# Optimization experiments

Hardware: AMD Instinct MI355X
Metric: run time of the kernel (lower is better)

The kernel has to match this reference:

```python
import jax, jax.numpy as jnp
import numpy as np

B, C, RXD, E, P, OSIZE = 64, 4, 64, 512, 4, 256


def setup_inputs() -> dict:
    key = jax.random.key(0)
    ks = jax.random.split(key, 6)
    x = jax.random.normal(ks[0], (B, C, RXD, E), dtype=jnp.float32)
    # rxd permutation (gather form of the one-hot permuteRxdMatrix matmul)
    rxd_perm = jax.random.permutation(ks[1], RXD)
    # E permutation and its compositions: permuter = permuter @ permuteEMatrix
    # in column-index form: idx_{p+1}[j] = idx_p[e_perm[j]]
    e_perm = np.array(jax.random.permutation(ks[2], E))
    idx = e_perm.copy()
    cols = []
    for _ in range(P):
        cols.append(idx.copy())
        idx = idx[e_perm]
    e_idx = jnp.asarray(np.stack(cols, axis=1))  # (E, P) int
    # sign selected at the single nonzero entry of each permutation column
    signs = (jax.random.uniform(ks[3], (E, P)) > 0.5).astype(jnp.float32) * 2.0 - 1.0
    fan_in = RXD * E * P
    W = jax.random.normal(ks[4], (OSIZE, fan_in), dtype=jnp.float32) / np.float32(np.sqrt(fan_in))
    b = jax.random.normal(ks[5], (OSIZE,), dtype=jnp.float32) * 0.01
    return {"x": x, "rxd_perm": rxd_perm, "e_idx": e_idx, "signs": signs, "W": W, "b": b}


def reference(x, rxd_perm, e_idx, signs, W, b):
    Bb, Cc, R, Ee = x.shape
    Pp = e_idx.shape[1]
    # permute rxd axis (exact equivalent of x.transpose @ one-hot matrix)
    out = x[:, :, rxd_perm, :]                      # (B,C,R,E)
    # signed E-permutations for all P powers (exact equiv of dense matmul
    # with permuteETensor * signTensor, which has one signed nonzero per column)
    out = out[..., e_idx] * signs                   # (B,C,R,E,P)
    L = R * Ee
    pieces = []
    for p in range(Pp):
        k = 2 ** p
        v = out[..., p].reshape(Bb, Cc, L)
        if k == 1:
            pieces.append(v)                        # pool+unpool with k=1 is identity
        else:
            Lp = ((L + k - 1) // k) * k             # ceil_mode padding
            vp = jnp.pad(v, ((0, 0), (0, 0), (0, Lp - L)), constant_values=-jnp.inf)
            w = vp.reshape(Bb, Cc, Lp // k, k)
            am = jnp.argmax(w, axis=-1)             # first max, matching torch MaxPool1d
            mx = jnp.max(w, axis=-1)
            onehot = jnp.arange(k) == am[..., None]
            # MaxUnpool: max value at argmax position, zeros elsewhere
            pieces.append(jnp.where(onehot, mx[..., None], 0.0).reshape(Bb, Cc, Lp))
    pieces[-1] = pieces[-1][:, :, :L]               # truncate last piece to L
    cat = jnp.concatenate(pieces, axis=2)           # (B,C,L*P) since L % k == 0
    return cat @ W.T + b                            # (B,C,OSIZE)
```

## Files before the change

### kernel.cpp

```cpp
#include <hip/hip_runtime.h>
#include <stdint.h>

#define B_ 64
#define C_ 4
#define R_ 64
#define E_ 512
#define P_ 4
#define OS_ 256
#define L_ (R_*E_)
#define K_ (L_*P_)
#define M_ (B_*C_)

#define BM 128
#define BN 128
#define BK 32
#define KCH 2048
#define AS_STR 40
#define WS_STR 36

typedef float  floatx4 __attribute__((ext_vector_type(4)));
typedef short  shortx8 __attribute__((ext_vector_type(8)));

static __device__ __forceinline__ unsigned short f2bf(float f) {
  union { float f; unsigned int u; } v; v.f = f;
  unsigned int u = v.u;
  u += 0x7fffu + ((u >> 16) & 1u);
  return (unsigned short)(u >> 16);
}

__global__ __launch_bounds__(512) void build_A(
    const float* __restrict__ x, const int* __restrict__ rxd_perm,
    const int* __restrict__ e_idx, const float* __restrict__ signs,
    unsigned short* __restrict__ A) {
  const int bcr = blockIdx.x;
  const int r  = bcr & (R_ - 1);
  const int bc = bcr >> 6;
  const int e  = threadIdx.x;
  __shared__ float xr[E_];
  __shared__ float vbuf[E_];
  const int pr = rxd_perm[r];
  xr[e] = x[((size_t)bc * R_ + pr) * E_ + e];
  __syncthreads();
  #pragma unroll
  for (int p = 0; p < P_; ++p) {
    const float v = xr[e_idx[e * P_ + p]] * signs[e * P_ + p];
    vbuf[e] = v;
    __syncthreads();
    float outv = v;
    if (p > 0) {
      const int k = 1 << p;
      const int base = e & ~(k - 1);
      float m = vbuf[base]; int am = base;
      for (int j = 1; j < k; ++j) {
        float t = vbuf[base + j];
        if (t > m) { m = t; am = base + j; }
      }
      outv = (e == am) ? v : 0.0f;
    }
    A[(size_t)bc * K_ + (size_t)p * L_ + r * E_ + e] = f2bf(outv);
    __syncthreads();
  }
}

__global__ void init_out(const float* __restrict__ bias, float* __restrict__ out) {
  const int i = blockIdx.x * blockDim.x + threadIdx.x;
  out[i] = bias[i & (OS_ - 1)];
}

__global__ __launch_bounds__(256) void gemm_splitk(
    const unsigned short* __restrict__ A, const float* __restrict__ W,
    float* __restrict__ out) {
  __shared__ unsigned short As[BM * AS_STR];
  __shared__ float Ws[BN * WS_STR];
  const int t    = threadIdx.x;
  const int lane = t & 63;
  const int wv   = t >> 6;
  const int mBase = blockIdx.x * BM;
  const int nBase = blockIdx.y * BN;
  const int k0base = blockIdx.z * KCH;

  const int wm   = (wv >> 1) * 64;
  const int wn   = (wv & 1) * 64;
  const int lrow = lane & 15;
  const int quad = lane >> 4;
  const int ks   = quad * 8;

  floatx4 acc[4][4];
  #pragma unroll
  for (int i = 0; i < 4; ++i)
    #pragma unroll
    for (int j = 0; j < 4; ++j)
      acc[i][j] = {0.f, 0.f, 0.f, 0.f};

  for (int kk = 0; kk < KCH; kk += BK) {
    const int k0 = k0base + kk;
    #pragma unroll
    for (int i = 0; i < 2; ++i) {
      const int fc = i * 256 + t;
      const int row = fc >> 2, ch = fc & 3;
      uint4 d = *(const uint4*)(A + (size_t)(mBase + row) * K_ + k0 + ch * 8);
      *(uint4*)(As + row * AS_STR + ch * 8) = d;
    }
    #pragma unroll
    for (int i = 0; i < 4; ++i) {
      const int fc = i * 256 + t;
      const int row = fc >> 3, ch = fc & 7;
      float4 d = *(const float4*)(W + (size_t)(nBase + row) * K_ + k0 + ch * 4);
      *(float4*)(Ws + row * WS_STR + ch * 4) = d;
    }
    __syncthreads();

    shortx8 af[4];
    #pragma unroll
    for (int ti = 0; ti < 4; ++ti)
      af[ti] = *(const shortx8*)(As + (wm + ti * 16 + lrow) * AS_STR + ks);

    #pragma unroll
    for (int tj = 0; tj < 4; ++tj) {
      const float* wrow = Ws + (wn + tj * 16 + lrow) * WS_STR + ks;
      const float4 w0 = *(const float4*)(wrow);
      const float4 w1 = *(const float4*)(wrow + 4);
      shortx8 bf;
      bf[0] = (short)f2bf(w0.x); bf[1] = (short)f2bf(w0.y);
      bf[2] = (short)f2bf(w0.z); bf[3] = (short)f2bf(w0.w);
      bf[4] = (short)f2bf(w1.x); bf[5] = (short)f2bf(w1.y);
      bf[6] = (short)f2bf(w1.z); bf[7] = (short)f2bf(w1.w);
      #pragma unroll
      for (int ti = 0; ti < 4; ++ti)
        acc[ti][tj] = __builtin_amdgcn_mfma_f32_16x16x32_bf16(af[ti], bf, acc[ti][tj], 0, 0, 0);
    }
    __syncthreads();
  }

  #pragma unroll
  for (int ti = 0; ti < 4; ++ti)
    #pragma unroll
    for (int tj = 0; tj < 4; ++tj)
      #pragma unroll
      for (int j = 0; j < 4; ++j) {
        const int m = mBase + wm + ti * 16 + quad * 4 + j;
        const int n = nBase + wn + tj * 16 + lrow;
        atomicAdd(out + (size_t)m * OS_ + n, acc[ti][tj][j]);
      }
}

extern "C" void kernel_launch(void* const* d_in, const int* in_sizes, int n_in,
                              void* d_out, int out_size, void* d_ws, size_t ws_size,
                              hipStream_t stream) {
  const float* x        = (const float*)d_in[0];
  const int*   rxd_perm = (const int*)d_in[1];
  const int*   e_idx    = (const int*)d_in[2];
  const float* signs    = (const float*)d_in[3];
  const float* W        = (const float*)d_in[4];
  const float* bias     = (const float*)d_in[5];
  float* out = (float*)d_out;
  unsigned short* A = (unsigned short*)d_ws;

  build_A<<<dim3(B_ * C_ * R_), dim3(512), 0, stream>>>(x, rxd_perm, e_idx, signs, A);
  init_out<<<dim3((OS_ * M_) / 256), dim3(256), 0, stream>>>(bias, out);
  gemm_splitk<<<dim3(M_ / BM, OS_ / BN, K_ / KCH), dim3(256), 0, stream>>>(A, W, out);
}
```

Before: 320.5 us.

## Rewrite build_A with shuffles, swizzle bf16 LDS tiles, replace atomics with partial-sum reduce

build_A now loads e_idx and signs as vectors and computes the max-pool argmax with wavefront shuffles instead of looping over shared memory behind barriers. The GEMM converts W to bf16 once when staging it into LDS, stores both tiles in an XOR-swizzled layout, and adds a launch-bounds occupancy hint. When the workspace is large enough, split-K partials go to a buffer and a separate reduce kernel adds them together with the bias, replacing atomics. This costs extra workspace memory and a larger split count, and keeps the atomic path as a fallback.

```diff
diff --git a/kernel.cpp b/kernel.cpp
--- a/kernel.cpp
+++ b/kernel.cpp
@@ -14,9 +14,6 @@
 #define BM 128
 #define BN 128
 #define BK 32
-#define KCH 2048
-#define AS_STR 40
-#define WS_STR 36
 
 typedef float  floatx4 __attribute__((ext_vector_type(4)));
 typedef short  shortx8 __attribute__((ext_vector_type(8)));
@@ -26,6 +23,10 @@
   unsigned int u = v.u;
   u += 0x7fffu + ((u >> 16) & 1u);
   return (unsigned short)(u >> 16);
+}
+
+static __device__ __forceinline__ int gidx(int row, int ch) {
+  return (row >> 4) * 64 + ch * 16 + ((row & 15) ^ (ch << 2));
 }
 
 __global__ __launch_bounds__(512) void build_A(
@@ -37,28 +38,45 @@
   const int bc = bcr >> 6;
   const int e  = threadIdx.x;
   __shared__ float xr[E_];
-  __shared__ float vbuf[E_];
-  const int pr = rxd_perm[r];
-  xr[e] = x[((size_t)bc * R_ + pr) * E_ + e];
+  xr[e] = x[((size_t)(bc * R_ + rxd_perm[r])) * E_ + e];
   __syncthreads();
-  #pragma unroll
-  for (int p = 0; p < P_; ++p) {
-    const float v = xr[e_idx[e * P_ + p]] * signs[e * P_ + p];
-    vbuf[e] = v;
-    __syncthreads();
-    float outv = v;
-    if (p > 0) {
-      const int k = 1 << p;
-      const int base = e & ~(k - 1);
-      float m = vbuf[base]; int am = base;
-      for (int j = 1; j < k; ++j) {
-        float t = vbuf[base + j];
-        if (t > m) { m = t; am = base + j; }
-      }
-      outv = (e == am) ? v : 0.0f;
-    }
-    A[(size_t)bc * K_ + (size_t)p * L_ + r * E_ + e] = f2bf(outv);
-    __syncthreads();
+
+  const uint4  ei = *(const uint4*)(e_idx + e * 4);
+  const float4 sg = *(const float4*)(signs + e * 4);
+  const float v0 = xr[ei.x] * sg.x;
+  const float v1 = xr[ei.y] * sg.y;
+  const float v2 = xr[ei.z] * sg.z;
+  const float v3 = xr[ei.w] * sg.w;
+
+  unsigned short* dst = A + (size_t)bc * K_ + r * E_ + e;
+  dst[0] = f2bf(v0);
+
+  {
+    const float ov = __shfl_xor(v1, 1, 64);
+    const bool keep = (e & 1) ? (v1 > ov) : (v1 >= ov);
+    dst[L_] = f2bf(keep ? v1 : 0.0f);
+  }
+  {
+    float m = v2; int mi = e;
+    #pragma unroll
+    for (int d = 1; d <= 2; d <<= 1) {
+      const float om  = __shfl_xor(m, d, 64);
+      const int   omi = __shfl_xor(mi, d, 64);
+      const bool take = (om > m) || (om == m && omi < mi);
+      m = take ? om : m; mi = take ? omi : mi;
+    }
+    dst[2 * L_] = f2bf((mi == e) ? v2 : 0.0f);
+  }
+  {
+    float m = v3; int mi = e;
+    #pragma unroll
+    for (int d = 1; d <= 4; d <<= 1) {
+      const float om  = __shfl_xor(m, d, 64);
+      const int   omi = __shfl_xor(mi, d, 64);
+      const bool take = (om > m) || (om == m && omi < mi);
+      m = take ? om : m; mi = take ? omi : mi;
+    }
+    dst[3 * L_] = f2bf((mi == e) ? v3 : 0.0f);
   }
 }
 
@@ -67,23 +85,24 @@
   out[i] = bias[i & (OS_ - 1)];
 }
 
-__global__ __launch_bounds__(256) void gemm_splitk(
+__global__ __launch_bounds__(256, 4) void gemm_splitk(
     const unsigned short* __restrict__ A, const float* __restrict__ W,
-    float* __restrict__ out) {
-  __shared__ unsigned short As[BM * AS_STR];
-  __shared__ float Ws[BN * WS_STR];
+    float* __restrict__ out, int kch, int atomic_mode) {
+  __shared__ unsigned short As[BM * BK];
+  __shared__ unsigned short Ws[BN * BK];
   const int t    = threadIdx.x;
   const int lane = t & 63;
   const int wv   = t >> 6;
   const int mBase = blockIdx.x * BM;
   const int nBase = blockIdx.y * BN;
-  const int k0base = blockIdx.z * KCH;
+  const size_t k0base = (size_t)blockIdx.z * kch;
 
   const int wm   = (wv >> 1) * 64;
   const int wn   = (wv & 1) * 64;
   const int lrow = lane & 15;
   const int quad = lane >> 4;
-  const int ks   = quad * 8;
+  const int srow = t >> 2;
+  const int sch  = t & 3;
 
   floatx4 acc[4][4];
   #pragma unroll
@@ -92,56 +111,84 @@
     for (int j = 0; j < 4; ++j)
       acc[i][j] = {0.f, 0.f, 0.f, 0.f};
 
-  for (int kk = 0; kk < KCH; kk += BK) {
-    const int k0 = k0base + kk;
+  for (int kk = 0; kk < kch; kk += BK) {
+    const size_t k0 = k0base + kk;
     #pragma unroll
     for (int i = 0; i < 2; ++i) {
-      const int fc = i * 256 + t;
-      const int row = fc >> 2, ch = fc & 3;
-      uint4 d = *(const uint4*)(A + (size_t)(mBase + row) * K_ + k0 + ch * 8);
-      *(uint4*)(As + row * AS_STR + ch * 8) = d;
-    }
-    #pragma unroll
-    for (int i = 0; i < 4; ++i) {
-      const int fc = i * 256 + t;
-      const int row = fc >> 3, ch = fc & 7;
-      float4 d = *(const float4*)(W + (size_t)(nBase + row) * K_ + k0 + ch * 4);
-      *(float4*)(Ws + row * WS_STR + ch * 4) = d;
+      const int rr = srow + i * 64;
+      const uint4 d = *(const uint4*)(A + (size_t)(mBase + rr) * K_ + k0 + sch * 8);
+      *(uint4*)(As + gidx(rr, sch) * 8) = d;
+    }
+    #pragma unroll
+    for (int i = 0; i < 2; ++i) {
+      const int rr = srow + i * 64;
+      const float* wp = W + (size_t)(nBase + rr) * K_ + k0 + sch * 8;
+      const float4 a0 = *(const float4*)(wp);
+      const float4 a1 = *(const float4*)(wp + 4);
+      shortx8 bfv;
+      bfv[0] = (short)f2bf(a0.x); bfv[1] = (short)f2bf(a0.y);
+      bfv[2] = (short)f2bf(a0.z); bfv[3] = (short)f2bf(a0.w);
+      bfv[4] = (short)f2bf(a1.x); bfv[5] = (short)f2bf(a1.y);
+      bfv[6] = (short)f2bf(a1.z); bfv[7] = (short)f2bf(a1.w);
+      *(shortx8*)(Ws + gidx(rr, sch) * 8) = bfv;
     }
     __syncthreads();
 
-    shortx8 af[4];
-    #pragma unroll
-    for (int ti = 0; ti < 4; ++ti)
-      af[ti] = *(const shortx8*)(As + (wm + ti * 16 + lrow) * AS_STR + ks);
-
-    #pragma unroll
-    for (int tj = 0; tj < 4; ++tj) {
-      const float* wrow = Ws + (wn + tj * 16 + lrow) * WS_STR + ks;
-      const float4 w0 = *(const float4*)(wrow);
-      const float4 w1 = *(const float4*)(wrow + 4);
-      shortx8 bf;
-      bf[0] = (short)f2bf(w0.x); bf[1] = (short)f2bf(w0.y);
-      bf[2] = (short)f2bf(w0.z); bf[3] = (short)f2bf(w0.w);
-      bf[4] = (short)f2bf(w1.x); bf[5] = (short)f2bf(w1.y);
-      bf[6] = (short)f2bf(w1.z); bf[7] = (short)f2bf(w1.w);
+    shortx8 af[4], wf[4];
+    const int fofs = quad * 16 + (lrow ^ (quad << 2));
+    #pragma unroll
+    for (int ti = 0; ti < 4; ++ti)
+      af[ti] = *(const shortx8*)(As + (((wm >> 4) + ti) * 64 + fofs) * 8);
+    #pragma unroll
+    for (int tj = 0; tj < 4; ++tj)
+      wf[tj] = *(const shortx8*)(Ws + (((wn >> 4) + tj) * 64 + fofs) * 8);
+
+    #pragma unroll
+    for (int ti = 0; ti < 4; ++ti)
       #pragma unroll
-      for (int ti = 0; ti < 4; ++ti)
-        acc[ti][tj] = __builtin_amdgcn_mfma_f32_16x16x32_bf16(af[ti], bf, acc[ti][tj], 0, 0, 0);
-    }
+      for (int tj = 0; tj < 4; ++tj)
+        acc[ti][tj] = __builtin_amdgcn_mfma_f32_16x16x32_bf16(af[ti], wf[tj], acc[ti][tj], 0, 0, 0);
     __syncthreads();
   }
 
-  #pragma unroll
-  for (int ti = 0; ti < 4; ++ti)
-    #pragma unroll
-    for (int tj = 0; tj < 4; ++tj)
+  if (atomic_mode == 0) {
+    float* dst = out + (size_t)blockIdx.z * (M_ * OS_);
+    #pragma unroll
+    for (int ti = 0; ti < 4; ++ti)
       #pragma unroll
-      for (int j = 0; j < 4; ++j) {
-        const int m = mBase + wm + ti * 16 + quad * 4 + j;
-        const int n = nBase + wn + tj * 16 + lrow;
-        atomicAdd(out + (size_t)m * OS_ + n, acc[ti][tj][j]);
-      }
+      for (int tj = 0; tj < 4; ++tj)
+        #pragma unroll
+        for (int j = 0; j < 4; ++j) {
+          const int m = mBase + wm + ti * 16 + quad * 4 + j;
+          const int n = nBase + wn + tj * 16 + lrow;
+          dst[(size_t)m * OS_ + n] = acc[ti][tj][j];
+        }
+  } else {
+    #pragma unroll
+    for (int ti = 0; ti < 4; ++ti)
+      #pragma unroll
+      for (int tj = 0; tj < 4; ++tj)
+        #pragma unroll
+        for (int j = 0; j < 4; ++j) {
+          const int m = mBase + wm + ti * 16 + quad * 4 + j;
+          const int n = nBase + wn + tj * 16 + lrow;
+          atomicAdd(out + (size_t)m * OS_ + n, acc[ti][tj][j]);
+        }
+  }
+}
+
+__global__ __launch_bounds__(256) void reduce_out(
+    const float* __restrict__ P, const float* __restrict__ bias,
+    float* __restrict__ out, int nz) {
+  const int tid = blockIdx.x * 256 + threadIdx.x;
+  const int n4 = (tid & 63) * 4;
+  const int m  = tid >> 6;
+  floatx4 s = *(const floatx4*)(bias + n4);
+  const float* p = P + (size_t)m * OS_ + n4;
+  #pragma unroll 8
+  for (int z = 0; z < nz; ++z)
+    s += *(const floatx4*)(p + (size_t)z * (M_ * OS_));
+  *(floatx4*)(out + (size_t)m * OS_ + n4) = s;
 }
 
 extern "C" void kernel_launch(void* const* d_in, const int* in_sizes, int n_in,
@@ -154,9 +201,21 @@
   const float* W        = (const float*)d_in[4];
   const float* bias     = (const float*)d_in[5];
   float* out = (float*)d_out;
+
   unsigned short* A = (unsigned short*)d_ws;
+  const size_t A_BYTES = (size_t)M_ * K_ * 2;
+  const int ZP = 256;
+  const size_t P_BYTES = (size_t)ZP * M_ * OS_ * 4;
+  float* Ppart = (float*)((char*)d_ws + A_BYTES);
+  const bool use_part = ws_size >= A_BYTES + P_BYTES;
 
   build_A<<<dim3(B_ * C_ * R_), dim3(512), 0, stream>>>(x, rxd_perm, e_idx, signs, A);
-  init_out<<<dim3((OS_ * M_) / 256), dim3(256), 0, stream>>>(bias, out);
-  gemm_splitk<<<dim3(M_ / BM, OS_ / BN, K_ / KCH), dim3(256), 0, stream>>>(A, W, out);
-}
+
+  if (use_part) {
+    gemm_splitk<<<dim3(M_ / BM, OS_ / BN, ZP), dim3(256), 0, stream>>>(A, W, Ppart, K_ / ZP, 0);
+    reduce_out<<<dim3(64), dim3(256), 0, stream>>>(Ppart, bias, out, ZP);
+  } else {
+    init_out<<<dim3((OS_ * M_) / 256), dim3(256), 0, stream>>>(bias, out);
+    gemm_splitk<<<dim3(M_ / BM, OS_ / BN, 128), dim3(256), 0, stream>>>(A, W, out, K_ / 128, 1);
+  }
+}
```

Measured after the change: 305.3 us. 4.7% less time.
